# Kernel optimization log

Measured on AMD Instinct MI355X. Metric: run time of the kernel, lower is better.

Reference implementation:

```python
import jax, jax.numpy as jnp
import numpy as np

N_NODES = 40000
N_EDGES = 640000
D_IN = 128
D_OUT = 128
BN_EPS = 1e-5


def setup_inputs() -> dict:
    key = jax.random.key(0)
    k1, k2, k3 = jax.random.split(key, 3)
    x = jax.random.normal(k1, (N_NODES, D_IN), dtype=jnp.float32)
    edge_index = jax.random.randint(k2, (2, N_EDGES), 0, N_NODES, dtype=jnp.int64)
    W = jax.random.normal(k3, (D_IN, D_OUT), dtype=jnp.float32) / np.sqrt(D_IN)
    b = jnp.zeros((D_OUT,), dtype=jnp.float32)
    gamma = jnp.ones((D_OUT,), dtype=jnp.float32)
    beta = jnp.zeros((D_OUT,), dtype=jnp.float32)
    return {"x": x, "edge_index": edge_index, "W": W, "b": b, "gamma": gamma, "beta": beta}


def reference(x, edge_index, W, b, gamma, beta):
    N = x.shape[0]
    # GCNConv (PyG semantics): add self-loops, symmetric normalization
    loop = jnp.arange(N, dtype=edge_index.dtype)
    src = jnp.concatenate([edge_index[0], loop])  # message sources
    dst = jnp.concatenate([edge_index[1], loop])  # scatter targets
    deg = jax.ops.segment_sum(jnp.ones_like(dst, dtype=x.dtype), dst, num_segments=N)
    dinv = jnp.where(deg > 0, deg ** -0.5, 0.0)
    norm = dinv[src] * dinv[dst]  # [E+N]
    h = x @ W  # [N, D_OUT] dense transform before propagation
    msgs = h[src] * norm[:, None]  # gather + scale, [E+N, D_OUT]
    out = jax.ops.segment_sum(msgs, dst, num_segments=N) + b
    # activation
    out = jax.nn.relu(out)
    # BatchNorm1d over node dim (training-mode batch statistics)
    mean = out.mean(axis=0)
    var = out.var(axis=0)
    out = (out - mean) * jax.lax.rsqrt(var + BN_EPS) * gamma + beta
    return out
```

## Files before the change

### kernel.cpp

```cpp
#include <hip/hip_runtime.h>
#include <math.h>

#define N_NODES 40000
#define N_EDGES 640000
#define D 128
#define BN_EPS 1e-5f
#define CAP 48
#define NBUCKET 64
#define SENT 40000

typedef __bf16 bf16x8 __attribute__((ext_vector_type(8)));
typedef unsigned short ushort8v __attribute__((ext_vector_type(8)));
typedef float floatx4 __attribute__((ext_vector_type(4)));

__device__ __forceinline__ unsigned bfr(float f) {
    unsigned b = __float_as_uint(f);
    return (b + 0x7fffu + ((b >> 16) & 1u)) >> 16;
}
__device__ __forceinline__ float4 bf4(uint2 u) {
    float4 r;
    r.x = __uint_as_float(u.x << 16);
    r.y = __uint_as_float(u.x & 0xffff0000u);
    r.z = __uint_as_float(u.y << 16);
    r.w = __uint_as_float(u.y & 0xffff0000u);
    return r;
}


__global__ __launch_bounds__(256) void k_init(int* __restrict__ cursor,
                                              float* __restrict__ smulti,
                                              unsigned* __restrict__ zrow,
                                              unsigned short* __restrict__ csr,
                                              const float* __restrict__ W,
                                              unsigned short* __restrict__ Wt) {
    int i = blockIdx.x * 256 + threadIdx.x;
    const unsigned sv = 0x9C409C40u;
    if (i < (N_NODES * CAP) / 8)
        ((uint4*)csr)[i] = make_uint4(sv, sv, sv, sv);
    if (i < N_NODES) cursor[i] = 0;
    if (i < NBUCKET * 256) smulti[i] = 0.0f;
    if (i < 64) zrow[i] = 0u;
    if (i < D * D) {
        int k = i >> 7, c = i & 127;
        Wt[c * D + k] = (unsigned short)bfr(W[i]);
    }
}


__global__ __launch_bounds__(256) void k_fill(const int* __restrict__ src,
                                              const int* __restrict__ dst,
                                              int* __restrict__ cursor,
                                              unsigned short* __restrict__ csr) {
    int e = blockIdx.x * 256 + threadIdx.x;
    if (e < N_EDGES) {
        int d = dst[e];
        int slot = atomicAdd(&cursor[d], 1);
        if (slot < CAP) csr[d * CAP + slot] = (unsigned short)src[e];
    }
}


__global__ __launch_bounds__(256) void k_gemm(const float* __restrict__ x,
                                              const unsigned short* __restrict__ Wt,
                                              const int* __restrict__ cursor,
                                              unsigned short* __restrict__ hp) {
    __shared__ unsigned short hs[64 * D];
    int wave = threadIdx.x >> 6;
    int lane = threadIdx.x & 63;
    int lm = lane & 15;
    int lg = lane >> 4;
    int r0 = blockIdx.x * 64 + wave * 16;

    bf16x8 a[4];
    const float* xrow = x + (size_t)(r0 + lm) * D;
#pragma unroll
    for (int ks = 0; ks < 4; ++ks) {
        int k0 = ks * 32 + lg * 8;
        float4 u0 = *(const float4*)(xrow + k0);
        float4 u1 = *(const float4*)(xrow + k0 + 4);
        ushort8v av;
        av[0] = (unsigned short)bfr(u0.x); av[1] = (unsigned short)bfr(u0.y);
        av[2] = (unsigned short)bfr(u0.z); av[3] = (unsigned short)bfr(u0.w);
        av[4] = (unsigned short)bfr(u1.x); av[5] = (unsigned short)bfr(u1.y);
        av[6] = (unsigned short)bfr(u1.z); av[7] = (unsigned short)bfr(u1.w);
        a[ks] = __builtin_bit_cast(bf16x8, av);
    }
    float dv[4];
#pragma unroll
    for (int j = 0; j < 4; ++j)
        dv[j] = rsqrtf((float)(cursor[r0 + lg * 4 + j] + 1));

#pragma unroll
    for (int nt = 0; nt < 8; ++nt) {
        floatx4 acc = {0.f, 0.f, 0.f, 0.f};
        const unsigned short* wrow = Wt + (size_t)(nt * 16 + lm) * D;
#pragma unroll
        for (int ks = 0; ks < 4; ++ks) {
            int k0 = ks * 32 + lg * 8;
            bf16x8 b = __builtin_bit_cast(bf16x8, *(const ushort8v*)(wrow + k0));
            acc = __builtin_amdgcn_mfma_f32_16x16x32_bf16(a[ks], b, acc, 0, 0, 0);
        }
#pragma unroll
        for (int j = 0; j < 4; ++j)
            hs[(wave * 16 + lg * 4 + j) * D + nt * 16 + lm] =
                (unsigned short)bfr(acc[j] * dv[j]);
    }
    __syncthreads();
    const uint4* hs4 = (const uint4*)hs;
    uint4* out4 = (uint4*)(hp + (size_t)blockIdx.x * 64 * D);
#pragma unroll
    for (int i = 0; i < 4; ++i)
        out4[i * 256 + threadIdx.x] = hs4[i * 256 + threadIdx.x];
}


__global__ __launch_bounds__(256) void k_gather(const unsigned short* __restrict__ hp,
                                                const int* __restrict__ cursor,
                                                const unsigned short* __restrict__ csr,
                                                const float* __restrict__ bvec,
                                                float* __restrict__ y,
                                                float* __restrict__ smulti) {
    const uint2* h2 = (const uint2*)hp;
    float4* y4 = (float4*)y;
    int c = threadIdx.x & 31;
    int g = threadIdx.x >> 5;
    float4 b4 = ((const float4*)bvec)[c];

    int n = blockIdx.x * 8 + g;
    float4 acc = bf4(h2[(size_t)n * 32 + c]);
    int cnt = cursor[n];
    const unsigned short* seg = csr + n * CAP;
    for (int j = 0; j < cnt; j += 8) {
        uint4 sv = *(const uint4*)(seg + j);
        int s0 = sv.x & 0xffff, s1 = sv.x >> 16;
        int s2 = sv.y & 0xffff, s3 = sv.y >> 16;
        int s4 = sv.z & 0xffff, s5 = sv.z >> 16;
        int s6 = sv.w & 0xffff, s7 = sv.w >> 16;
        uint2 u0 = h2[(size_t)s0 * 32 + c];
        uint2 u1 = h2[(size_t)s1 * 32 + c];
        uint2 u2 = h2[(size_t)s2 * 32 + c];
        uint2 u3 = h2[(size_t)s3 * 32 + c];
        uint2 u4 = h2[(size_t)s4 * 32 + c];
        uint2 u5 = h2[(size_t)s5 * 32 + c];
        uint2 u6 = h2[(size_t)s6 * 32 + c];
        uint2 u7 = h2[(size_t)s7 * 32 + c];
        float4 v0 = bf4(u0), v1 = bf4(u1), v2 = bf4(u2), v3 = bf4(u3);
        float4 v4 = bf4(u4), v5 = bf4(u5), v6 = bf4(u6), v7 = bf4(u7);
        acc.x += ((v0.x + v1.x) + (v2.x + v3.x)) + ((v4.x + v5.x) + (v6.x + v7.x));
        acc.y += ((v0.y + v1.y) + (v2.y + v3.y)) + ((v4.y + v5.y) + (v6.y + v7.y));
        acc.z += ((v0.z + v1.z) + (v2.z + v3.z)) + ((v4.z + v5.z) + (v6.z + v7.z));
        acc.w += ((v0.w + v1.w) + (v2.w + v3.w)) + ((v4.w + v5.w) + (v6.w + v7.w));
    }
    float di = rsqrtf((float)(cnt + 1));
    float4 o;
    o.x = fmaxf(fmaf(acc.x, di, b4.x), 0.f);
    o.y = fmaxf(fmaf(acc.y, di, b4.y), 0.f);
    o.z = fmaxf(fmaf(acc.z, di, b4.z), 0.f);
    o.w = fmaxf(fmaf(acc.w, di, b4.w), 0.f);
    y4[(size_t)n * 32 + c] = o;

    float4 sum = o;
    float4 ssq;
    ssq.x = o.x * o.x; ssq.y = o.y * o.y; ssq.z = o.z * o.z; ssq.w = o.w * o.w;

    __shared__ float4 s1m[256], s2m[256];
    s1m[threadIdx.x] = sum;
    s2m[threadIdx.x] = ssq;
    __syncthreads();
    if (threadIdx.x < 32) {
        float4 a = s1m[threadIdx.x], b = s2m[threadIdx.x];
#pragma unroll
        for (int g2 = 1; g2 < 8; ++g2) {
            float4 p = s1m[g2 * 32 + threadIdx.x], q = s2m[g2 * 32 + threadIdx.x];
            a.x += p.x; a.y += p.y; a.z += p.z; a.w += p.w;
            b.x += q.x; b.y += q.y; b.z += q.z; b.w += q.w;
        }
        float* sb = smulti + (blockIdx.x & (NBUCKET - 1)) * 256;
        int d0 = 4 * threadIdx.x;
        atomicAdd(&sb[d0 + 0], a.x); atomicAdd(&sb[d0 + 1], a.y);
        atomicAdd(&sb[d0 + 2], a.z); atomicAdd(&sb[d0 + 3], a.w);
        atomicAdd(&sb[128 + d0 + 0], b.x); atomicAdd(&sb[128 + d0 + 1], b.y);
        atomicAdd(&sb[128 + d0 + 2], b.z); atomicAdd(&sb[128 + d0 + 3], b.w);
    }
}


__global__ __launch_bounds__(256) void k_bnfinal(float* __restrict__ y,
                                                 const float* __restrict__ smulti,
                                                 const float* __restrict__ gamma,
                                                 const float* __restrict__ beta) {
    __shared__ float sc[128], bi[128];
    {
        int t = threadIdx.x;
        float s = 0.f;
#pragma unroll 8
        for (int k = 0; k < NBUCKET; ++k) s += smulti[k * 256 + t];
        __shared__ float stats[256];
        stats[t] = s;
        __syncthreads();
        if (t < 128) {
            float invN = 1.0f / (float)N_NODES;
            float mean = stats[t] * invN;
            float var = stats[128 + t] * invN - mean * mean;
            float rs = rsqrtf(var + BN_EPS) * gamma[t];
            sc[t] = rs;
            bi[t] = beta[t] - mean * rs;
        }
    }
    __syncthreads();
    const int total = N_NODES * 32;
    for (int idx = blockIdx.x * 256 + threadIdx.x; idx < total;
         idx += gridDim.x * 256) {
        int c = idx & 31;
        float4 v = ((const float4*)y)[idx];
        int d0 = 4 * c;
        v.x = fmaf(v.x, sc[d0 + 0], bi[d0 + 0]);
        v.y = fmaf(v.y, sc[d0 + 1], bi[d0 + 1]);
        v.z = fmaf(v.z, sc[d0 + 2], bi[d0 + 2]);
        v.w = fmaf(v.w, sc[d0 + 3], bi[d0 + 3]);
        ((float4*)y)[idx] = v;
    }
}

extern "C" void kernel_launch(void* const* d_in, const int* in_sizes, int n_in,
                              void* d_out, int out_size, void* d_ws, size_t ws_size,
                              hipStream_t stream) {
    const float* x     = (const float*)d_in[0];
    const int*   ei    = (const int*)d_in[1];
    const float* W     = (const float*)d_in[2];
    const float* bvec  = (const float*)d_in[3];
    const float* gamma = (const float*)d_in[4];
    const float* beta  = (const float*)d_in[5];
    float* y = (float*)d_out;

    const int* src = ei;
    const int* dst = ei + N_EDGES;

    char* ws = (char*)d_ws;
    unsigned short* hp = (unsigned short*)ws;
    size_t off = (size_t)(N_NODES + 1) * D * 2;
    unsigned short* Wt = (unsigned short*)(ws + off);
    off += D * D * 2;
    float* smulti = (float*)(ws + off);
    off += NBUCKET * 256 * 4;
    int* cursor = (int*)(ws + off);
    off += (size_t)N_NODES * 4;
    unsigned short* csr = (unsigned short*)(ws + off);

    k_init<<<938, 256, 0, stream>>>(cursor, smulti,
                                    (unsigned*)(hp + (size_t)N_NODES * D), csr, W, Wt);
    k_fill<<<(N_EDGES + 255) / 256, 256, 0, stream>>>(src, dst, cursor, csr);
    k_gemm<<<N_NODES / 64, 256, 0, stream>>>(x, Wt, cursor, hp);
    k_gather<<<N_NODES / 8, 256, 0, stream>>>(hp, cursor, csr, bvec, y, smulti);
    k_bnfinal<<<160, 256, 0, stream>>>(y, smulti, gamma, beta);
}
```

Baseline: 112.5 us.

## Build CSR via two-pass binned partition instead of global per-node atomics

```diff
diff --git a/kernel.cpp b/kernel.cpp
--- a/kernel.cpp
+++ b/kernel.cpp
@@ -7,7 +7,10 @@
 #define BN_EPS 1e-5f
 #define CAP 48
 #define NBUCKET 64
-#define SENT 40000
+#define NB 250
+#define BINW 160
+#define EP 2500
+#define PCAP 4096
 
 typedef __bf16 bf16x8 __attribute__((ext_vector_type(8)));
 typedef unsigned short ushort8v __attribute__((ext_vector_type(8)));
@@ -27,36 +30,87 @@
 }
 
 
-__global__ __launch_bounds__(256) void k_init(int* __restrict__ cursor,
+__global__ __launch_bounds__(256) void k_init(int* __restrict__ gcur,
                                               float* __restrict__ smulti,
                                               unsigned* __restrict__ zrow,
-                                              unsigned short* __restrict__ csr,
                                               const float* __restrict__ W,
                                               unsigned short* __restrict__ Wt) {
     int i = blockIdx.x * 256 + threadIdx.x;
-    const unsigned sv = 0x9C409C40u;
-    if (i < (N_NODES * CAP) / 8)
-        ((uint4*)csr)[i] = make_uint4(sv, sv, sv, sv);
-    if (i < N_NODES) cursor[i] = 0;
-    if (i < NBUCKET * 256) smulti[i] = 0.0f;
+    if (i < NB) gcur[i] = 0;
+    smulti[i] = 0.0f;
     if (i < 64) zrow[i] = 0u;
-    if (i < D * D) {
+    {
         int k = i >> 7, c = i & 127;
         Wt[c * D + k] = (unsigned short)bfr(W[i]);
     }
 }
 
 
-__global__ __launch_bounds__(256) void k_fill(const int* __restrict__ src,
+__global__ __launch_bounds__(256) void k_part(const int* __restrict__ src,
                                               const int* __restrict__ dst,
-                                              int* __restrict__ cursor,
-                                              unsigned short* __restrict__ csr) {
-    int e = blockIdx.x * 256 + threadIdx.x;
-    if (e < N_EDGES) {
-        int d = dst[e];
-        int slot = atomicAdd(&cursor[d], 1);
-        if (slot < CAP) csr[d * CAP + slot] = (unsigned short)src[e];
-    }
+                                              int* __restrict__ gcur,
+                                              unsigned* __restrict__ pbuf) {
+    __shared__ int lcnt[NB];
+    __shared__ int lbase[NB];
+    __shared__ unsigned short epk[EP];
+    int t = threadIdx.x;
+    for (int i = t; i < NB; i += 256) lcnt[i] = 0;
+    __syncthreads();
+    int e0 = blockIdx.x * EP;
+    for (int r = 0; r < EP; r += 256) {
+        if (r + t < EP) {
+            int d = dst[e0 + r + t];
+            int bin = d / BINW;
+            epk[r + t] = (unsigned short)((bin << 8) | (d - bin * BINW));
+            atomicAdd(&lcnt[bin], 1);
+        }
+    }
+    __syncthreads();
+    for (int i = t; i < NB; i += 256) {
+        lbase[i] = atomicAdd(&gcur[i], lcnt[i]);
+        lcnt[i] = 0;
+    }
+    __syncthreads();
+    for (int r = 0; r < EP; r += 256) {
+        if (r + t < EP) {
+            unsigned short ep = epk[r + t];
+            int bin = ep >> 8, dl = ep & 255;
+            int rank = atomicAdd(&lcnt[bin], 1);
+            int pos = lbase[bin] + rank;
+            if (pos < PCAP)
+                pbuf[bin * PCAP + pos] =
+                    (unsigned)src[e0 + r + t] | ((unsigned)dl << 16);
+        }
+    }
+}
+
+
+__global__ __launch_bounds__(256) void k_binfill(const unsigned* __restrict__ pbuf,
+                                                 const int* __restrict__ gcur,
+                                                 unsigned short* __restrict__ csr,
+                                                 int* __restrict__ cursor) {
+    __shared__ int cur[BINW];
+    __shared__ unsigned short stage[BINW * CAP];
+    int t = threadIdx.x;
+    int bin = blockIdx.x;
+    for (int i = t; i < BINW; i += 256) cur[i] = 0;
+    const unsigned sv = 0x9C409C40u;
+    for (int i = t; i < (BINW * CAP) / 2; i += 256) ((unsigned*)stage)[i] = sv;
+    __syncthreads();
+    int ne = min(gcur[bin], PCAP);
+    const unsigned* pb = pbuf + bin * PCAP;
+    for (int i = t; i < ne; i += 256) {
+        unsigned p = pb[i];
+        int dl = p >> 16, s = p & 0xffff;
+        int slot = atomicAdd(&cur[dl], 1);
+        if (slot < CAP) stage[dl * CAP + slot] = (unsigned short)s;
+    }
+    __syncthreads();
+    unsigned* dc = (unsigned*)(csr + (size_t)bin * BINW * CAP);
+    const unsigned* st = (const unsigned*)stage;
+    for (int i = t; i < (BINW * CAP) / 2; i += 256) dc[i] = st[i];
+    for (int i = t; i < BINW; i += 256)
+        cursor[bin * BINW + i] = min(cur[i], CAP);
 }
 
 
@@ -129,7 +183,7 @@
     int n = blockIdx.x * 8 + g;
     float4 acc = bf4(h2[(size_t)n * 32 + c]);
     int cnt = cursor[n];
-    const unsigned short* seg = csr + n * CAP;
+    const unsigned short* seg = csr + (size_t)n * CAP;
     for (int j = 0; j < cnt; j += 8) {
         uint4 sv = *(const uint4*)(seg + j);
         int s0 = sv.x & 0xffff, s1 = sv.x >> 16;
@@ -246,10 +300,15 @@
     int* cursor = (int*)(ws + off);
     off += (size_t)N_NODES * 4;
     unsigned short* csr = (unsigned short*)(ws + off);
-
-    k_init<<<938, 256, 0, stream>>>(cursor, smulti,
-                                    (unsigned*)(hp + (size_t)N_NODES * D), csr, W, Wt);
-    k_fill<<<(N_EDGES + 255) / 256, 256, 0, stream>>>(src, dst, cursor, csr);
+    off += (size_t)N_NODES * CAP * 2;
+    int* gcur = (int*)(ws + off);
+    off += (size_t)((NB + 63) & ~63) * 4;
+    unsigned* pbuf = (unsigned*)(ws + off);
+
+    k_init<<<64, 256, 0, stream>>>(gcur, smulti,
+                                   (unsigned*)(hp + (size_t)N_NODES * D), W, Wt);
+    k_part<<<N_EDGES / EP, 256, 0, stream>>>(src, dst, gcur, pbuf);
+    k_binfill<<<NB, 256, 0, stream>>>(pbuf, gcur, csr, cursor);
     k_gemm<<<N_NODES / 64, 256, 0, stream>>>(x, Wt, cursor, hp);
     k_gather<<<N_NODES / 8, 256, 0, stream>>>(hp, cursor, csr, bvec, y, smulti);
     k_bnfinal<<<160, 256, 0, stream>>>(y, smulti, gamma, beta);
```

New measurement: 94.29 us. 1.19x faster.
